# Performance work log

Measured on AMD Instinct MI355X. Metric: run time of the kernel, lower is better.

Reference implementation:

```python
import jax, jax.numpy as jnp
import numpy as np

B, L, M = 32768, 128, 1024  # batch, latent_size, num_basis_function


def setup_inputs() -> dict:
    key = jax.random.key(0)
    k1, k2, k3 = jax.random.split(key, 3)
    u_lat = jax.random.normal(k1, (B, L), dtype=jnp.float32)
    centres = jax.random.normal(k2, (M, L), dtype=jnp.float32)      # RBF centres (torch init: N(0,1))
    log_sigmas = jnp.zeros((M,), dtype=jnp.float32)                  # RBF log bandwidths (torch init: 0)
    lin1_w = jax.random.normal(k3, (M,), dtype=jnp.float32) / np.float32(np.sqrt(M))  # Linear(M,1,bias=False)
    return {"u_lat": u_lat, "centres": centres, "log_sigmas": log_sigmas, "lin1_w": lin1_w}


def _V_batch(u, centres, log_sigmas, lin1_w):
    """Potential V(h) = ELU(w . multiquadric(||h-c||/sigma)) + 0.5*||h||^2, per row. Returns [B]."""
    u_sq = jnp.sum(u * u, axis=-1)                                   # [B]
    c_sq = jnp.sum(centres * centres, axis=-1)                       # [M]
    # ||h - c||^2 via norm expansion: avoids [B, M, L] intermediate
    sq_dist = jnp.maximum(u_sq[:, None] + c_sq[None, :] - 2.0 * (u @ centres.T), 0.0)  # [B, M]
    d = jnp.sqrt(sq_dist) / jnp.exp(log_sigmas)[None, :]             # [B, M]
    phi = jnp.sqrt(1.0 + d * d)                                      # multiquadric kernel
    e = jax.nn.elu(phi @ lin1_w)                                     # [B]
    return e + 0.5 * u_sq


def reference(u_lat, centres, log_sigmas, lin1_w):
    # LEBNN.forward: f_lat = dV/dh evaluated per sample (vmap(jacrev) in torch).
    # Each entry of _V_batch depends only on its own row of u_lat, so
    # grad of the summed potential gives the per-sample Jacobian rows exactly.
    grad_fn = jax.grad(lambda u: jnp.sum(_V_batch(u, centres, log_sigmas, lin1_w)))
    return grad_fn(u_lat)  # [B, L]
```

## Files before the change

kernel.cpp:

```cpp
#include <hip/hip_runtime.h>
#include <math.h>

#define B_N 32768
#define L_N 128
#define M_N 1024
#define NT 512
#define TB 64
#define TM 64
#define NCHUNK (M_N / TM)

typedef __bf16 v8bf __attribute__((ext_vector_type(8)));
typedef __bf16 v4bf __attribute__((ext_vector_type(4)));
typedef float  v4f  __attribute__((ext_vector_type(4)));
typedef float  v2f  __attribute__((ext_vector_type(2)));
typedef unsigned int u32x2 __attribute__((ext_vector_type(2)));

#define MFMA(a, b, c) __builtin_amdgcn_mfma_f32_16x16x32_bf16(a, b, c, 0, 0, 0)

#define US  136
#define CNS 136
#define QSCALE 64.0f
#define QINV   0.015625f

__device__ inline v8bf pack8(float4 a, float4 b) {
    v8bf v;
    v[0] = (__bf16)a.x; v[1] = (__bf16)a.y; v[2] = (__bf16)a.z; v[3] = (__bf16)a.w;
    v[4] = (__bf16)b.x; v[5] = (__bf16)b.y; v[6] = (__bf16)b.z; v[7] = (__bf16)b.w;
    return v;
}

__global__ void lebnn_setup(const float* __restrict__ centres,
                            const float* __restrict__ log_sigmas,
                            const float* __restrict__ lin_w,
                            float4* __restrict__ cpack,
                            __bf16* __restrict__ cT,
                            __bf16* __restrict__ cbn) {
    __shared__ __bf16 tile[64 * 72];
    const int bx = blockIdx.x;
    if (bx < 32) {
        const int m0 = (bx & 15) * 64;
        const int l0 = (bx >> 4) * 64;
        const int row = threadIdx.x >> 2;
        const int seg = threadIdx.x & 3;
        const float* src = centres + (size_t)(m0 + row) * L_N + l0 + seg * 16;
        float4 a0 = *(const float4*)(src);
        float4 a1 = *(const float4*)(src + 4);
        float4 a2 = *(const float4*)(src + 8);
        float4 a3 = *(const float4*)(src + 12);
        v8bf p0 = pack8(a0, a1);
        v8bf p1 = pack8(a2, a3);
        *(v8bf*)&tile[row * 72 + seg * 16]     = p0;
        *(v8bf*)&tile[row * 72 + seg * 16 + 8] = p1;
        __bf16* rdst = cbn + (size_t)(m0 + row) * L_N + l0 + seg * 16;
        *(v8bf*)(rdst)     = p0;
        *(v8bf*)(rdst + 8) = p1;
        __syncthreads();
        v8bf o0, o1;
#pragma unroll
        for (int i = 0; i < 8; ++i) o0[i] = tile[(seg * 16 + i) * 72 + row];
#pragma unroll
        for (int i = 0; i < 8; ++i) o1[i] = tile[(seg * 16 + 8 + i) * 72 + row];
        __bf16* dst = cT + (size_t)(l0 + row) * M_N + m0 + seg * 16;
        *(v8bf*)(dst)     = o0;
        *(v8bf*)(dst + 8) = o1;
    } else {
        int m = (bx - 32) * 256 + threadIdx.x;
        if (m < M_N) {
            const float4* row = (const float4*)(centres + (size_t)m * L_N);
            float s = 0.f;
#pragma unroll
            for (int i = 0; i < L_N / 4; ++i) {
                float4 v = row[i];
                s += v.x * v.x + v.y * v.y + v.z * v.z + v.w * v.w;
            }
            float4 p;
            p.x = s;
            p.y = expf(-2.f * log_sigmas[m]);
            p.z = lin_w[m];
            p.w = 0.f;
            cpack[m] = p;
        }
    }
}

__global__ __launch_bounds__(NT) void lebnn_phase1(
    const float* __restrict__ u, const __bf16* __restrict__ cbn,
    const float4* __restrict__ cpack, unsigned int* __restrict__ qg32,
    float* __restrict__ gg, float* __restrict__ rsg)
{
    __shared__ __bf16 u_bf[TB * US];
    __shared__ __bf16 c_n[TM * CNS];
    __shared__ float usq_s[TB];
    __shared__ float upart[TB * 9];
    __shared__ float sred[288];
    __shared__ float rred[288];

    const int tid  = threadIdx.x;
    const int w    = tid >> 6;
    const int lane = tid & 63;
    const int l15  = lane & 15;
    const int l4   = lane >> 4;
    const int bh   = w >> 2;
    const int mq   = w & 3;
    const int b0   = blockIdx.x * TB;

    {
        int row = tid >> 3, seg = tid & 7;
        const float* up = u + (size_t)(b0 + row) * L_N + seg * 16;
        float4 a0 = *(const float4*)(up);
        float4 a1 = *(const float4*)(up + 4);
        float4 a2 = *(const float4*)(up + 8);
        float4 a3 = *(const float4*)(up + 12);
        float ps = a0.x*a0.x + a0.y*a0.y + a0.z*a0.z + a0.w*a0.w
                 + a1.x*a1.x + a1.y*a1.y + a1.z*a1.z + a1.w*a1.w
                 + a2.x*a2.x + a2.y*a2.y + a2.z*a2.z + a2.w*a2.w
                 + a3.x*a3.x + a3.y*a3.y + a3.z*a3.z + a3.w*a3.w;
        *(v8bf*)&u_bf[row * US + seg * 16]     = pack8(a0, a1);
        *(v8bf*)&u_bf[row * US + seg * 16 + 8] = pack8(a2, a3);
        upart[row * 9 + seg] = ps;
    }
    __syncthreads();
    if (tid < TB) {
        float s = 0.f;
#pragma unroll
        for (int i = 0; i < 8; ++i) s += upart[tid * 9 + i];
        usq_s[tid] = s;
    }
    __syncthreads();

    v8bf uf[2][4];
#pragma unroll
    for (int bt = 0; bt < 2; ++bt)
#pragma unroll
        for (int kk = 0; kk < 4; ++kk)
            uf[bt][kk] = *(v8bf*)&u_bf[(bh*32 + bt*16 + l15) * US + kk*32 + l4*8];

    float usq_r[2][4];
#pragma unroll
    for (int bt = 0; bt < 2; ++bt)
#pragma unroll
        for (int r = 0; r < 4; ++r)
            usq_r[bt][r] = usq_s[bh*32 + bt*16 + l4*4 + r];

    float s_p[2][4] = {{0.f,0.f,0.f,0.f},{0.f,0.f,0.f,0.f}};
    float r_p[2][4] = {{0.f,0.f,0.f,0.f},{0.f,0.f,0.f,0.f}};

    const int srow = tid >> 3;
    const int sseg = tid & 7;

    v8bf lda, ldb;
    {
        const __bf16* cp = cbn + (size_t)srow * L_N + sseg * 16;
        lda = *(const v8bf*)(cp);
        ldb = *(const v8bf*)(cp + 8);
    }

    for (int mt = 0; mt < NCHUNK; ++mt) {
        const int m0 = mt * TM;
        __syncthreads();
        *(v8bf*)&c_n[srow * CNS + sseg * 16]     = lda;
        *(v8bf*)&c_n[srow * CNS + sseg * 16 + 8] = ldb;
        float4 cpv = cpack[m0 + mq*16 + l15];
        __syncthreads();

        if (mt + 1 < NCHUNK) {
            const __bf16* cp = cbn + (size_t)((mt+1)*TM + srow) * L_N + sseg * 16;
            lda = *(const v8bf*)(cp);
            ldb = *(const v8bf*)(cp + 8);
        }

        v4f dot[2];
        dot[0] = (v4f){0.f,0.f,0.f,0.f};
        dot[1] = (v4f){0.f,0.f,0.f,0.f};
#pragma unroll
        for (int kk = 0; kk < 4; ++kk) {
            v8bf bfr = *(v8bf*)&c_n[(mq*16 + l15) * CNS + kk*32 + l4*8];
            dot[0] = MFMA(uf[0][kk], bfr, dot[0]);
            dot[1] = MFMA(uf[1][kk], bfr, dot[1]);
        }

        float qs[8];
        const float wqs = cpv.z * cpv.y * QSCALE;
#pragma unroll
        for (int bt = 0; bt < 2; ++bt) {
#pragma unroll
            for (int r = 0; r < 4; ++r) {
                float dv  = dot[bt][r];
                float raw = fmaf(-2.f, dv, usq_r[bt][r] + cpv.x);
                float x   = fmaf(fmaxf(raw, 0.f), cpv.y, 1.f);
                float ri  = rsqrtf(x);
                s_p[bt][r] = fmaf(cpv.z, x * ri, s_p[bt][r]);
                float qv  = (raw > 0.f) ? wqs * ri : 0.f;
                r_p[bt][r] += qv;
                qs[bt*4 + r] = qv;
            }
        }
        unsigned int w0 = 0, w1 = 0;
        w0 = __builtin_amdgcn_cvt_pk_fp8_f32(qs[0], qs[1], w0, false);
        w0 = __builtin_amdgcn_cvt_pk_fp8_f32(qs[2], qs[3], w0, true);
        w1 = __builtin_amdgcn_cvt_pk_fp8_f32(qs[4], qs[5], w1, false);
        w1 = __builtin_amdgcn_cvt_pk_fp8_f32(qs[6], qs[7], w1, true);
        u32x2 qw; qw[0] = w0; qw[1] = w1;
        *(u32x2*)(qg32 + ((size_t)blockIdx.x * NCHUNK + mt) * (NT * 2) + tid * 2) = qw;
    }

#pragma unroll
    for (int bt = 0; bt < 2; ++bt)
#pragma unroll
        for (int r = 0; r < 4; ++r) {
#pragma unroll
            for (int msk = 1; msk < 16; msk <<= 1) {
                s_p[bt][r] += __shfl_xor(s_p[bt][r], msk, 64);
                r_p[bt][r] += __shfl_xor(r_p[bt][r], msk, 64);
            }
        }
    if (l15 == 0) {
#pragma unroll
        for (int bt = 0; bt < 2; ++bt)
#pragma unroll
            for (int r = 0; r < 4; ++r) {
                sred[w*36 + bt*16 + l4*4 + r] = s_p[bt][r];
                rred[w*36 + bt*16 + l4*4 + r] = r_p[bt][r];
            }
    }
    __syncthreads();

    if (tid < TB) {
        int bhh = tid >> 5, rowr = tid & 31;
        float s = 0.f, R = 0.f;
#pragma unroll
        for (int i = 0; i < 4; ++i) {
            s += sred[(bhh*4 + i)*36 + rowr];
            R += rred[(bhh*4 + i)*36 + rowr];
        }
        float g = (s > 0.f) ? 1.f : expf(s);
        gg[b0 + tid]  = g;
        rsg[b0 + tid] = fmaf(g * QINV, R, 1.f);
    }
}

__global__ __launch_bounds__(NT) void lebnn_gemm2(
    const float* __restrict__ u, const unsigned int* __restrict__ qg32,
    const __bf16* __restrict__ cT, const float* __restrict__ gg,
    const float* __restrict__ rsg, float* __restrict__ out)
{
    __shared__ __bf16 qt[64 * 72];
    __shared__ __bf16 ct[128 * 72];

    const int tid  = threadIdx.x;
    const int w    = tid >> 6;
    const int lane = tid & 63;
    const int l15  = lane & 15;
    const int l4   = lane >> 4;
    const int bh   = w >> 2;
    const int lq   = w & 3;
    const int bb0  = blockIdx.x * 64;
    const int lr   = tid >> 2;
    const int sg   = tid & 3;

    v4f acc[2][2];
#pragma unroll
    for (int bt = 0; bt < 2; ++bt)
#pragma unroll
        for (int lt = 0; lt < 2; ++lt)
            acc[bt][lt] = (v4f){0.f, 0.f, 0.f, 0.f};

    u32x2 qw = *(const u32x2*)(qg32 + ((size_t)blockIdx.x * NCHUNK + 0) * (NT * 2) + tid * 2);
    const __bf16* csrc = cT + (size_t)lr * M_N + sg * 16;
    v8bf cva = *(const v8bf*)(csrc);
    v8bf cvb = *(const v8bf*)(csrc + 8);

    for (int mt = 0; mt < NCHUNK; ++mt) {
        __syncthreads();
        {
            v2f p0 = __builtin_amdgcn_cvt_pk_f32_fp8(qw[0], false);
            v2f p1 = __builtin_amdgcn_cvt_pk_f32_fp8(qw[0], true);
            v2f p2 = __builtin_amdgcn_cvt_pk_f32_fp8(qw[1], false);
            v2f p3 = __builtin_amdgcn_cvt_pk_f32_fp8(qw[1], true);
            __bf16 qb[8];
            qb[0] = (__bf16)p0[0]; qb[1] = (__bf16)p0[1];
            qb[2] = (__bf16)p1[0]; qb[3] = (__bf16)p1[1];
            qb[4] = (__bf16)p2[0]; qb[5] = (__bf16)p2[1];
            qb[6] = (__bf16)p3[0]; qb[7] = (__bf16)p3[1];
#pragma unroll
            for (int bt = 0; bt < 2; ++bt)
#pragma unroll
                for (int r = 0; r < 4; ++r)
                    qt[(bh*32 + bt*16 + l4*4 + r) * 72 + lq*16 + l15] = qb[bt*4 + r];
            *(v8bf*)&ct[lr * 72 + sg * 16]     = cva;
            *(v8bf*)&ct[lr * 72 + sg * 16 + 8] = cvb;
        }
        __syncthreads();

        if (mt + 1 < NCHUNK) {
            qw = *(const u32x2*)(qg32 + ((size_t)blockIdx.x * NCHUNK + (mt+1)) * (NT * 2) + tid * 2);
            const __bf16* cn = cT + (size_t)lr * M_N + (mt+1) * TM + sg * 16;
            cva = *(const v8bf*)(cn);
            cvb = *(const v8bf*)(cn + 8);
        }

#pragma unroll
        for (int kk = 0; kk < 2; ++kk) {
            v8bf qa0 = *(v8bf*)&qt[(bh*32 +  0 + l15) * 72 + kk*32 + l4*8];
            v8bf qa1 = *(v8bf*)&qt[(bh*32 + 16 + l15) * 72 + kk*32 + l4*8];
#pragma unroll
            for (int lt = 0; lt < 2; ++lt) {
                v8bf cb = *(v8bf*)&ct[(lq*32 + lt*16 + l15) * 72 + kk*32 + l4*8];
                acc[0][lt] = MFMA(qa0, cb, acc[0][lt]);
                acc[1][lt] = MFMA(qa1, cb, acc[1][lt]);
            }
        }
    }

    float gv[2][4], rv[2][4];
#pragma unroll
    for (int bt = 0; bt < 2; ++bt)
#pragma unroll
        for (int r = 0; r < 4; ++r) {
            int b = bb0 + bh*32 + bt*16 + l4*4 + r;
            gv[bt][r] = gg[b] * QINV;
            rv[bt][r] = rsg[b];
        }
#pragma unroll
    for (int bt = 0; bt < 2; ++bt)
#pragma unroll
        for (int lt = 0; lt < 2; ++lt)
#pragma unroll
            for (int r = 0; r < 4; ++r) {
                size_t idx = (size_t)(bb0 + bh*32 + bt*16 + l4*4 + r) * L_N
                           + lq*32 + lt*16 + l15;
                out[idx] = fmaf(u[idx], rv[bt][r], -gv[bt][r] * acc[bt][lt][r]);
            }
}

#define CFS 68
#define OFF_UBF   0
#define OFF_CN    17408
#define OFF_CFL   34816
#define OFF_USQ   52224
#define OFF_UPART 52480
#define OFF_SRED  54784
#define OFF_RRED  55936
#define OFF_G     57088
#define OFF_RS    57344
#define SMEM_BYTES 57600

__global__ __launch_bounds__(NT) void lebnn_fallback(
    const float* __restrict__ u, const float* __restrict__ centres,
    const float4* __restrict__ cpack, float* __restrict__ out)
{
    extern __shared__ char smem[];
    __bf16* u_bf = (__bf16*)(smem + OFF_UBF);
    __bf16* c_n  = (__bf16*)(smem + OFF_CN);
    float*  cfl  = (float*)(smem + OFF_CFL);
    float* usq_s = (float*)(smem + OFF_USQ);
    float* upart = (float*)(smem + OFF_UPART);
    float* sred  = (float*)(smem + OFF_SRED);
    float* rred  = (float*)(smem + OFF_RRED);
    float* gsh   = (float*)(smem + OFF_G);
    float* rssh  = (float*)(smem + OFF_RS);

    const int tid  = threadIdx.x;
    const int w    = tid >> 6;
    const int lane = tid & 63;
    const int l15  = lane & 15;
    const int l4   = lane >> 4;
    const int bh   = w >> 2;
    const int mq   = w & 3;
    const int tx   = tid & 15;
    const int ty   = tid >> 4;
    const int b0   = blockIdx.x * 64;

    {
        int row = tid >> 3, seg = tid & 7;
        const float* up = u + (size_t)(b0 + row) * L_N + seg * 16;
        float4 a0 = *(const float4*)(up);
        float4 a1 = *(const float4*)(up + 4);
        float4 a2 = *(const float4*)(up + 8);
        float4 a3 = *(const float4*)(up + 12);
        float ps = a0.x*a0.x + a0.y*a0.y + a0.z*a0.z + a0.w*a0.w
                 + a1.x*a1.x + a1.y*a1.y + a1.z*a1.z + a1.w*a1.w
                 + a2.x*a2.x + a2.y*a2.y + a2.z*a2.z + a2.w*a2.w
                 + a3.x*a3.x + a3.y*a3.y + a3.z*a3.z + a3.w*a3.w;
        *(v8bf*)&u_bf[row * US + seg * 16]     = pack8(a0, a1);
        *(v8bf*)&u_bf[row * US + seg * 16 + 8] = pack8(a2, a3);
        upart[row * 9 + seg] = ps;
    }
    __syncthreads();
    if (tid < 64) {
        float s = 0.f;
#pragma unroll
        for (int i = 0; i < 8; ++i) s += upart[tid * 9 + i];
        usq_s[tid] = s;
    }
    __syncthreads();

    v8bf uf[2][4];
#pragma unroll
    for (int bt = 0; bt < 2; ++bt)
#pragma unroll
        for (int kk = 0; kk < 4; ++kk)
            uf[bt][kk] = *(v8bf*)&u_bf[(bh*32 + bt*16 + l15) * US + kk*32 + l4*8];

    float usq_r[2][4];
#pragma unroll
    for (int bt = 0; bt < 2; ++bt)
#pragma unroll
        for (int r = 0; r < 4; ++r)
            usq_r[bt][r] = usq_s[bh*32 + bt*16 + l4*4 + r];

    float s_p[2][4] = {{0.f,0.f,0.f,0.f},{0.f,0.f,0.f,0.f}};
    float r_p[2][4] = {{0.f,0.f,0.f,0.f},{0.f,0.f,0.f,0.f}};
    float T[4][4] = {{0.f}};

    const int rp = tid >> 4;
    const int cg = tid & 15;

    for (int mt = 0; mt < NCHUNK; ++mt) {
        const int m0 = mt * TM;
        __syncthreads();
        {
            const float* cp0 = centres + (size_t)(m0 + 2*rp) * L_N + cg * 8;
            float4 r0a = *(const float4*)(cp0);
            float4 r0b = *(const float4*)(cp0 + 4);
            float4 r1a = *(const float4*)(cp0 + L_N);
            float4 r1b = *(const float4*)(cp0 + L_N + 4);
            *(v8bf*)&c_n[(2*rp)     * CNS + cg*8] = pack8(r0a, r0b);
            *(v8bf*)&c_n[(2*rp + 1) * CNS + cg*8] = pack8(r1a, r1b);
        }
        float4 cpv = cpack[m0 + mq*16 + l15];
        __syncthreads();

        v4f dot[2];
        dot[0] = (v4f){0.f,0.f,0.f,0.f};
        dot[1] = (v4f){0.f,0.f,0.f,0.f};
#pragma unroll
        for (int kk = 0; kk < 4; ++kk) {
            v8bf bfr = *(v8bf*)&c_n[(mq*16 + l15) * CNS + kk*32 + l4*8];
            dot[0] = MFMA(uf[0][kk], bfr, dot[0]);
            dot[1] = MFMA(uf[1][kk], bfr, dot[1]);
        }

#pragma unroll
        for (int bt = 0; bt < 2; ++bt) {
#pragma unroll
            for (int r = 0; r < 4; ++r) {
                float dv  = dot[bt][r];
                float raw = fmaf(-2.f, dv, usq_r[bt][r] + cpv.x);
                float x   = fmaf(fmaxf(raw, 0.f), cpv.y, 1.f);
                float ri  = rsqrtf(x);
                s_p[bt][r] = fmaf(cpv.z, x * ri, s_p[bt][r]);
                float qv  = (raw > 0.f) ? cpv.z * cpv.y * ri : 0.f;
                r_p[bt][r] += qv;
                cfl[(mq*16 + l15) * CFS + bh*32 + bt*16 + l4*4 + r] = qv;
            }
        }
        __syncthreads();

        for (int mm = 0; mm < TM; ++mm) {
            v4f cf = *(v4f*)&cfl[mm * CFS + tx*4];
            v4bf cb = *(v4bf*)&c_n[mm * CNS + ty*4];
            float cv[4] = {(float)cb[0], (float)cb[1], (float)cb[2], (float)cb[3]};
#pragma unroll
            for (int i = 0; i < 4; ++i)
#pragma unroll
                for (int j = 0; j < 4; ++j)
                    T[i][j] = fmaf(cf[i], cv[j], T[i][j]);
        }
    }

    __syncthreads();

#pragma unroll
    for (int bt = 0; bt < 2; ++bt)
#pragma unroll
        for (int r = 0; r < 4; ++r) {
#pragma unroll
            for (int msk = 1; msk < 16; msk <<= 1) {
                s_p[bt][r] += __shfl_xor(s_p[bt][r], msk, 64);
                r_p[bt][r] += __shfl_xor(r_p[bt][r], msk, 64);
            }
        }
    if (l15 == 0) {
#pragma unroll
        for (int bt = 0; bt < 2; ++bt)
#pragma unroll
            for (int r = 0; r < 4; ++r) {
                sred[w*36 + bt*16 + l4*4 + r] = s_p[bt][r];
                rred[w*36 + bt*16 + l4*4 + r] = r_p[bt][r];
            }
    }
    __syncthreads();

    if (tid < 64) {
        int bhh = tid >> 5, rowr = tid & 31;
        float s = 0.f, R = 0.f;
#pragma unroll
        for (int i = 0; i < 4; ++i) {
            s += sred[(bhh*4 + i)*36 + rowr];
            R += rred[(bhh*4 + i)*36 + rowr];
        }
        float g = (s > 0.f) ? 1.f : expf(s);
        gsh[tid]  = g;
        rssh[tid] = fmaf(g, R, 1.f);
    }
    __syncthreads();

#pragma unroll
    for (int i = 0; i < 4; ++i) {
        int b = tx*4 + i;
        float rv = rssh[b];
        float gv = gsh[b];
        size_t idx = (size_t)(b0 + b) * L_N + ty*4;
        float4 uu = *(const float4*)(u + idx);
        float4 o;
        o.x = fmaf(uu.x, rv, -gv * T[i][0]);
        o.y = fmaf(uu.y, rv, -gv * T[i][1]);
        o.z = fmaf(uu.z, rv, -gv * T[i][2]);
        o.w = fmaf(uu.w, rv, -gv * T[i][3]);
        *(float4*)(out + idx) = o;
    }
}

extern "C" void kernel_launch(void* const* d_in, const int* in_sizes, int n_in,
                              void* d_out, int out_size, void* d_ws, size_t ws_size,
                              hipStream_t stream) {
    const float* u          = (const float*)d_in[0];
    const float* centres    = (const float*)d_in[1];
    const float* log_sigmas = (const float*)d_in[2];
    const float* lin_w      = (const float*)d_in[3];
    float* out = (float*)d_out;

    char* wsb = (char*)d_ws;
    float4* cpack = (float4*)wsb;
    __bf16* cT    = (__bf16*)(wsb + 16384);
    __bf16* cbn   = (__bf16*)(wsb + 278528);
    float*  gg    = (float*) (wsb + 540672);
    float*  rsg   = (float*) (wsb + 671744);
    unsigned int* qg32 = (unsigned int*)(wsb + 802816);
    const size_t WS_NEED = 802816ULL + 33554432ULL;

    lebnn_setup<<<36, 256, 0, stream>>>(centres, log_sigmas, lin_w, cpack, cT, cbn);

    if (ws_size >= WS_NEED) {
        lebnn_phase1<<<B_N / TB, NT, 0, stream>>>(u, cbn, cpack, qg32, gg, rsg);
        lebnn_gemm2<<<B_N / 64, NT, 0, stream>>>(u, qg32, cT, gg, rsg, out);
    } else {
        hipFuncSetAttribute((const void*)lebnn_fallback,
                            hipFuncAttributeMaxDynamicSharedMemorySize, SMEM_BYTES);
        lebnn_fallback<<<B_N / 64, NT, SMEM_BYTES, stream>>>(u, centres, cpack, out);
    }
}
```

Baseline: 63.39 us.

## Split phase1 over two M halves per batch tile and add finalize kernel

Phase1 now launches twice as many blocks, each covering half of the basis-function chunks for a 64-row batch tile, and writes partial s and R sums to new workspace buffers. A small finalize kernel combines the two halves and computes the ELU gate and row scale. The aim is more blocks in flight on the many CUs, with each block running a shorter loop. The cost is loading and converting the u tile twice, an extra kernel launch, and a larger workspace that may make the fast path fall back if the workspace is too small.

Result: slower. 77.77 us (+22.7%).

```diff
diff --git a/kernel.cpp b/kernel.cpp
--- a/kernel.cpp
+++ b/kernel.cpp
@@ -8,6 +8,7 @@
 #define TB 64
 #define TM 64
 #define NCHUNK (M_N / TM)
+#define NCH2 (NCHUNK / 2)
 
 typedef __bf16 v8bf __attribute__((ext_vector_type(8)));
 typedef __bf16 v4bf __attribute__((ext_vector_type(4)));
@@ -86,7 +87,7 @@
 __global__ __launch_bounds__(NT) void lebnn_phase1(
     const float* __restrict__ u, const __bf16* __restrict__ cbn,
     const float4* __restrict__ cpack, unsigned int* __restrict__ qg32,
-    float* __restrict__ gg, float* __restrict__ rsg)
+    float* __restrict__ sg_part, float* __restrict__ rg_part)
 {
     __shared__ __bf16 u_bf[TB * US];
     __shared__ __bf16 c_n[TM * CNS];
@@ -102,7 +103,10 @@
     const int l4   = lane >> 4;
     const int bh   = w >> 2;
     const int mq   = w & 3;
-    const int b0   = blockIdx.x * TB;
+    const int brow  = blockIdx.x >> 1;
+    const int mhalf = blockIdx.x & 1;
+    const int b0   = brow * TB;
+    const int ch0  = mhalf * NCH2;
 
     {
         int row = tid >> 3, seg = tid & 7;
@@ -150,21 +154,22 @@
 
     v8bf lda, ldb;
     {
-        const __bf16* cp = cbn + (size_t)srow * L_N + sseg * 16;
+        const __bf16* cp = cbn + (size_t)(ch0 * TM + srow) * L_N + sseg * 16;
         lda = *(const v8bf*)(cp);
         ldb = *(const v8bf*)(cp + 8);
     }
 
-    for (int mt = 0; mt < NCHUNK; ++mt) {
-        const int m0 = mt * TM;
+    for (int mt = 0; mt < NCH2; ++mt) {
+        const int ch = ch0 + mt;
+        const int m0 = ch * TM;
         __syncthreads();
         *(v8bf*)&c_n[srow * CNS + sseg * 16]     = lda;
         *(v8bf*)&c_n[srow * CNS + sseg * 16 + 8] = ldb;
         float4 cpv = cpack[m0 + mq*16 + l15];
         __syncthreads();
 
-        if (mt + 1 < NCHUNK) {
-            const __bf16* cp = cbn + (size_t)((mt+1)*TM + srow) * L_N + sseg * 16;
+        if (mt + 1 < NCH2) {
+            const __bf16* cp = cbn + (size_t)(m0 + TM + srow) * L_N + sseg * 16;
             lda = *(const v8bf*)(cp);
             ldb = *(const v8bf*)(cp + 8);
         }
@@ -201,7 +206,7 @@
         w1 = __builtin_amdgcn_cvt_pk_fp8_f32(qs[4], qs[5], w1, false);
         w1 = __builtin_amdgcn_cvt_pk_fp8_f32(qs[6], qs[7], w1, true);
         u32x2 qw; qw[0] = w0; qw[1] = w1;
-        *(u32x2*)(qg32 + ((size_t)blockIdx.x * NCHUNK + mt) * (NT * 2) + tid * 2) = qw;
+        *(u32x2*)(qg32 + ((size_t)brow * NCHUNK + ch) * (NT * 2) + tid * 2) = qw;
     }
 
 #pragma unroll
@@ -233,10 +238,21 @@
             s += sred[(bhh*4 + i)*36 + rowr];
             R += rred[(bhh*4 + i)*36 + rowr];
         }
-        float g = (s > 0.f) ? 1.f : expf(s);
-        gg[b0 + tid]  = g;
-        rsg[b0 + tid] = fmaf(g * QINV, R, 1.f);
-    }
+        sg_part[(size_t)mhalf * B_N + b0 + tid] = s;
+        rg_part[(size_t)mhalf * B_N + b0 + tid] = R;
+    }
+}
+
+__global__ __launch_bounds__(256) void lebnn_finalize(
+    const float* __restrict__ sg_part, const float* __restrict__ rg_part,
+    float* __restrict__ gg, float* __restrict__ rsg)
+{
+    int b = blockIdx.x * 256 + threadIdx.x;
+    float s = sg_part[b] + sg_part[B_N + b];
+    float R = rg_part[b] + rg_part[B_N + b];
+    float g = (s > 0.f) ? 1.f : expf(s);
+    gg[b]  = g;
+    rsg[b] = fmaf(g * QINV, R, 1.f);
 }
 
 __global__ __launch_bounds__(NT) void lebnn_gemm2(
@@ -538,12 +554,15 @@
     float*  gg    = (float*) (wsb + 540672);
     float*  rsg   = (float*) (wsb + 671744);
     unsigned int* qg32 = (unsigned int*)(wsb + 802816);
-    const size_t WS_NEED = 802816ULL + 33554432ULL;
+    float* sg_part = (float*)(wsb + 802816 + 33554432);
+    float* rg_part = (float*)(wsb + 802816 + 33554432 + 262144);
+    const size_t WS_NEED = 802816ULL + 33554432ULL + 524288ULL;
 
     lebnn_setup<<<36, 256, 0, stream>>>(centres, log_sigmas, lin_w, cpack, cT, cbn);
 
     if (ws_size >= WS_NEED) {
-        lebnn_phase1<<<B_N / TB, NT, 0, stream>>>(u, cbn, cpack, qg32, gg, rsg);
+        lebnn_phase1<<<(B_N / TB) * 2, NT, 0, stream>>>(u, cbn, cpack, qg32, sg_part, rg_part);
+        lebnn_finalize<<<B_N / 256, 256, 0, stream>>>(sg_part, rg_part, gg, rsg);
         lebnn_gemm2<<<B_N / 64, NT, 0, stream>>>(u, qg32, cT, gg, rsg, out);
     } else {
         hipFuncSetAttribute((const void*)lebnn_fallback,
```
